# Optimization experiments

Measured on AMD Instinct MI355X. Metric: run time of the kernel, lower is better.

## Reference

```python
import jax, jax.numpy as jnp
import numpy as np

N = 50000
E = 800000
D = 128
EPS = 1e-5


def setup_inputs() -> dict:
    key = jax.random.key(0)
    ks = jax.random.split(key, 12)
    x = jax.random.normal(ks[0], (N, D), dtype=jnp.float32)
    pos = jax.random.normal(ks[1], (N, 3), dtype=jnp.float32)
    edge_index = jax.random.randint(ks[2], (2, E), 0, N, dtype=jnp.int32)
    s_e1 = 1.0 / np.sqrt(2 * D + 1)
    s_d = 1.0 / np.sqrt(D)
    s_n1 = 1.0 / np.sqrt(2 * D)
    return {
        "x": x,
        "pos": pos,
        "edge_index": edge_index,
        "W1e": jax.random.uniform(ks[3], (2 * D + 1, D), jnp.float32, -s_e1, s_e1),
        "b1e": jnp.zeros((D,), jnp.float32),
        "W2e": jax.random.uniform(ks[4], (D, D), jnp.float32, -s_d, s_d),
        "b2e": jnp.zeros((D,), jnp.float32),
        "W1n": jax.random.uniform(ks[5], (2 * D, D), jnp.float32, -s_n1, s_n1),
        "b1n": jnp.zeros((D,), jnp.float32),
        "W2n": jax.random.uniform(ks[6], (D, D), jnp.float32, -s_d, s_d),
        "b2n": jnp.zeros((D,), jnp.float32),
        "gamma": jnp.ones((D,), jnp.float32),
        "beta": jnp.zeros((D,), jnp.float32),
    }


def reference(x, pos, edge_index, W1e, b1e, W2e, b2e, W1n, b1n, W2n, b2n, gamma, beta):
    row, col = edge_index[0], edge_index[1]
    # gather + relative position
    rel_pos = pos[row] - pos[col]                       # [E, 3]
    dist2 = jnp.sum(rel_pos * rel_pos, axis=1, keepdims=True)  # [E, 1]
    edge_input = jnp.concatenate([x[row], x[col], dist2], axis=1)  # [E, 2D+1]
    # 2-layer edge MLP with SiLU activations
    h = jax.nn.silu(edge_input @ W1e + b1e)
    edge_feat = jax.nn.silu(h @ W2e + b2e)              # [E, D]
    # scatter-add aggregation onto source nodes (row)
    agg = jax.ops.segment_sum(edge_feat, row, num_segments=x.shape[0])  # [N, D]
    # 2-layer node MLP (SiLU only after first layer)
    node_in = jnp.concatenate([x, agg], axis=1)         # [N, 2D]
    update = jax.nn.silu(node_in @ W1n + b1n) @ W2n + b2n
    # dropout omitted (inference/eval mode)
    # LayerNorm(x + update)
    y = x + update
    mu = jnp.mean(y, axis=-1, keepdims=True)
    var = jnp.var(y, axis=-1, keepdims=True)
    return (y - mu) * jax.lax.rsqrt(var + EPS) * gamma + beta
```

## Files before the change

### kernel.cpp

```cpp
#include <hip/hip_runtime.h>
#include <hip/hip_bf16.h>
#include <math.h>

#define D 128
#define NND 50000
#define NE 800000
#define NB1 196
#define TPITCH 152
#define CPITCH 132

typedef __attribute__((ext_vector_type(8))) short shortx8;
typedef __attribute__((ext_vector_type(4))) float floatx4;

__device__ __forceinline__ float silu_f(float v) {
    return v * __builtin_amdgcn_rcpf(1.0f + __expf(-v));
}
__device__ __forceinline__ unsigned short f2bf(float f) {
    union { float f; unsigned int u; } v; v.f = f;
    unsigned int u = v.u;
    u += 0x7fffu + ((u >> 16) & 1u);
    return (unsigned short)(u >> 16);
}
__device__ __forceinline__ void unpk(unsigned int u, float& lo, float& hi) {
    union { unsigned int x; float f; } a, b;
    a.x = u << 16;
    b.x = u & 0xffff0000u;
    lo = a.f; hi = b.f;
}

__global__ void zero_kernel(float4* __restrict__ p, int n4) {
    int i = blockIdx.x * blockDim.x + threadIdx.x;
    float4 z = make_float4(0.f, 0.f, 0.f, 0.f);
    for (; i < n4; i += gridDim.x * blockDim.x) p[i] = z;
}

__global__ void hist_kernel(const int* __restrict__ ei, int* __restrict__ deg) {
    int e = blockIdx.x * 256 + threadIdx.x;
    atomicAdd(&deg[ei[e]], 1);
}

__global__ void scan1_kernel(const int* __restrict__ deg,
                             int* __restrict__ part, int* __restrict__ bsum) {
    __shared__ int s[256];
    const int tid = threadIdx.x;
    const int i = blockIdx.x * 256 + tid;
    int v = (i < NND) ? deg[i] : 0;
    s[tid] = v;
    __syncthreads();
    #pragma unroll
    for (int off = 1; off < 256; off <<= 1) {
        int t = (tid >= off) ? s[tid - off] : 0;
        __syncthreads();
        s[tid] += t;
        __syncthreads();
    }
    part[i] = s[tid] - v;
    if (tid == 255) bsum[blockIdx.x] = s[255];
}

__global__ void scan2_kernel(const int* __restrict__ bsum, int* __restrict__ boff) {
    __shared__ int s[256];
    const int tid = threadIdx.x;
    int v = (tid < NB1) ? bsum[tid] : 0;
    s[tid] = v;
    __syncthreads();
    #pragma unroll
    for (int off = 1; off < 256; off <<= 1) {
        int t = (tid >= off) ? s[tid - off] : 0;
        __syncthreads();
        s[tid] += t;
        __syncthreads();
    }
    if (tid < NB1) boff[tid] = s[tid] - v;
}

__global__ void scan3_kernel(const int* __restrict__ part, const int* __restrict__ boff,
                             int* __restrict__ rowptr, int* __restrict__ cursor) {
    int i = blockIdx.x * 256 + threadIdx.x;
    if (i < NND) {
        int v = part[i] + boff[i >> 8];
        rowptr[i] = v;
        cursor[i] = v;
    } else if (i == NND) {
        rowptr[NND] = NE;
    }
}

__global__ void scatter_kernel(const int* __restrict__ ei, const float* __restrict__ pos,
                               int* __restrict__ cursor,
                               uint4* __restrict__ epack) {
    int e = blockIdx.x * 256 + threadIdx.x;
    int r = ei[e], c = ei[NE + e];
    float dx = pos[r * 3 + 0] - pos[c * 3 + 0];
    float dy = pos[r * 3 + 1] - pos[c * 3 + 1];
    float dz = pos[r * 3 + 2] - pos[c * 3 + 2];
    float d2 = dx * dx + dy * dy + dz * dz;
    int slot = atomicAdd(&cursor[r], 1);
    uint4 v;
    v.x = (unsigned int)c;
    v.y = (unsigned int)r;
    v.z = __float_as_uint(d2);
    v.w = 0u;
    epack[slot] = v;
}

__global__ void wswzall_kernel(const float* __restrict__ W1e, const float* __restrict__ W1n,
                               const float* __restrict__ W2e, const float* __restrict__ W2n,
                               unsigned short* __restrict__ w1f, unsigned short* __restrict__ w1nf,
                               unsigned short* __restrict__ w2f, unsigned short* __restrict__ w2nf,
                               unsigned short* __restrict__ wlf) {
    const int b = blockIdx.x;
    const float* W; unsigned short* Wf; int lb;
    if (b < 128)      { W = W1e; Wf = w1f;  lb = b; }
    else if (b < 256) { W = W1n; Wf = w1nf; lb = b - 128; }
    else if (b < 320) { W = W2e; Wf = w2f;  lb = b - 256; }
    else if (b < 384) { W = W2n; Wf = w2nf; lb = b - 320; }
    else {
        if (threadIdx.x < 128) wlf[threadIdx.x] = f2bf(W1e[256 * D + threadIdx.x]);
        return;
    }
    int f = lb * 256 + threadIdx.x;
    int j    = f & 7;
    int mrow = (f >> 3) & 15;
    int n    = (f >> 7) & 7;
    int rest = f >> 10;
    int quad = rest & 3;
    int ks   = rest >> 2;
    int col = n * 16 + mrow;
    int k   = ks * 32 + quad * 8 + j;
    Wf[f] = f2bf(W[k * D + col]);
}

__global__ __launch_bounds__(256) void precompute_kernel(
        const float* __restrict__ x,
        const unsigned short* __restrict__ w1f,
        const float* __restrict__ b1e,
        unsigned short* __restrict__ A,
        unsigned short* __restrict__ Bm) {
    const int t    = threadIdx.x;
    const int wv   = t >> 6;
    const int lane = t & 63;
    const int mrow = lane & 15;
    const int quad = lane >> 4;
    const int tile = blockIdx.x * 4 + wv;
    if (tile >= 3125) return;
    const int n0 = tile * 16;

    const float4* xrow = (const float4*)(x + ((size_t)(n0 + mrow) << 7));
    const uint4* wp   = (const uint4*)w1f;

    floatx4 accA[8], accB[8];
    #pragma unroll
    for (int n = 0; n < 8; ++n) {
        accA[n] = (floatx4){0.f, 0.f, 0.f, 0.f};
        accB[n] = (floatx4){0.f, 0.f, 0.f, 0.f};
    }

    #pragma unroll
    for (int s = 0; s < 4; ++s) {
        float4 xa = xrow[(s * 4 + quad) * 2 + 0];
        float4 xb = xrow[(s * 4 + quad) * 2 + 1];
        union { shortx8 v; __hip_bfloat162 p[4]; } af;
        af.p[0] = __float22bfloat162_rn(float2{xa.x, xa.y});
        af.p[1] = __float22bfloat162_rn(float2{xa.z, xa.w});
        af.p[2] = __float22bfloat162_rn(float2{xb.x, xb.y});
        af.p[3] = __float22bfloat162_rn(float2{xb.z, xb.w});
        const int baseA = (s * 4 + quad) * 128 + mrow;
        const int baseB = ((s + 4) * 4 + quad) * 128 + mrow;
        #pragma unroll
        for (int n = 0; n < 8; ++n) {
            union { uint4 u; shortx8 v; } bfA, bfB;
            bfA.u = wp[baseA + n * 16];
            bfB.u = wp[baseB + n * 16];
            accA[n] = __builtin_amdgcn_mfma_f32_16x16x32_bf16(af.v, bfA.v, accA[n], 0, 0, 0);
            accB[n] = __builtin_amdgcn_mfma_f32_16x16x32_bf16(af.v, bfB.v, accB[n], 0, 0, 0);
        }
    }

    float bb[8];
    #pragma unroll
    for (int n = 0; n < 8; ++n) bb[n] = b1e[n * 16 + mrow];

    #pragma unroll
    for (int reg = 0; reg < 4; ++reg) {
        const int node = n0 + quad * 4 + reg;
        #pragma unroll
        for (int n = 0; n < 8; ++n) {
            const int col = n * 16 + mrow;
            A[(size_t)node * D + col]  = f2bf(accA[n][reg] + bb[n]);
            Bm[(size_t)node * D + col] = f2bf(accB[n][reg]);
        }
    }
}

__global__ __launch_bounds__(256, 2) void edgered_kernel(
        const unsigned short* __restrict__ Abf,
        const unsigned short* __restrict__ Bbf,
        const uint4* __restrict__ epack,
        const unsigned short* __restrict__ wlf,
        const unsigned short* __restrict__ W2f,
        const float* __restrict__ b2e,
        float* __restrict__ hpart,
        float* __restrict__ tpart,
        float* __restrict__ aggf) {
    __shared__ float cs[64][CPITCH];
    __shared__ int   rn[64];

    const int t    = threadIdx.x;
    const int wv   = t >> 6;
    const int lane = t & 63;
    const int mrow = lane & 15;
    const int quad = lane >> 4;
    const int e0   = blockIdx.x * 64 + wv * 16;
    const int eme  = e0 + mrow;

    const uint4 ep = epack[eme];
    const int   c  = (int)ep.x;
    const int   r  = (int)ep.y;
    const float d2 = __uint_as_float(ep.z);

    const uint4* arow = (const uint4*)(Abf + ((size_t)r << 7));
    const uint4* brow = (const uint4*)(Bbf + ((size_t)c << 7));
    const uint4* wlq  = (const uint4*)wlf;
    const uint4* w2p  = (const uint4*)W2f;

    uint4 au[4], bu[4], wu[4];
    #pragma unroll
    for (int s = 0; s < 4; ++s) {
        au[s] = arow[s * 4 + quad];
        bu[s] = brow[s * 4 + quad];
        wu[s] = wlq[s * 4 + quad];
    }

    floatx4 acc[8];
    #pragma unroll
    for (int k = 0; k < 8; ++k) acc[k] = (floatx4){0.f, 0.f, 0.f, 0.f};

    #pragma unroll
    for (int s = 0; s < 4; ++s) {
        float a0, a1, a2, a3, a4, a5, a6, a7;
        float q0, q1, q2, q3, q4, q5, q6, q7;
        float w0, w1, w2, w3, w4, w5, w6, w7;
        unpk(au[s].x, a0, a1); unpk(au[s].y, a2, a3);
        unpk(au[s].z, a4, a5); unpk(au[s].w, a6, a7);
        unpk(bu[s].x, q0, q1); unpk(bu[s].y, q2, q3);
        unpk(bu[s].z, q4, q5); unpk(bu[s].w, q6, q7);
        unpk(wu[s].x, w0, w1); unpk(wu[s].y, w2, w3);
        unpk(wu[s].z, w4, w5); unpk(wu[s].w, w6, w7);

        float h0 = silu_f(fmaf(d2, w0, a0 + q0));
        float h1 = silu_f(fmaf(d2, w1, a1 + q1));
        float h2 = silu_f(fmaf(d2, w2, a2 + q2));
        float h3 = silu_f(fmaf(d2, w3, a3 + q3));
        float h4 = silu_f(fmaf(d2, w4, a4 + q4));
        float h5 = silu_f(fmaf(d2, w5, a5 + q5));
        float h6 = silu_f(fmaf(d2, w6, a6 + q6));
        float h7 = silu_f(fmaf(d2, w7, a7 + q7));

        union { shortx8 v; __hip_bfloat162 p[4]; } af;
        af.p[0] = __float22bfloat162_rn(float2{h0, h1});
        af.p[1] = __float22bfloat162_rn(float2{h2, h3});
        af.p[2] = __float22bfloat162_rn(float2{h4, h5});
        af.p[3] = __float22bfloat162_rn(float2{h6, h7});

        const int base = (s * 4 + quad) * 128 + mrow;
        #pragma unroll
        for (int k = 0; k < 8; ++k) {
            union { uint4 u; shortx8 v; } bf;
            bf.u = w2p[base + k * 16];
            acc[k] = __builtin_amdgcn_mfma_f32_16x16x32_bf16(af.v, bf.v, acc[k], 0, 0, 0);
        }
    }

    float bias[8];
    #pragma unroll
    for (int k = 0; k < 8; ++k) bias[k] = b2e[k * 16 + mrow];

    #pragma unroll
    for (int reg = 0; reg < 4; ++reg) {
        const int row = wv * 16 + quad * 4 + reg;
        #pragma unroll
        for (int k = 0; k < 8; ++k)
            cs[row][k * 16 + mrow] = silu_f(acc[k][reg] + bias[k]);
    }
    if (lane < 16) rn[wv * 16 + lane] = r;
    __syncthreads();

    if (wv < 2) {
        const int col = wv * 64 + lane;
        const size_t blk = blockIdx.x;
        int i = 0;
        while (i < 64) {
            const int n = rn[i];
            int j = i + 1;
            while (j < 64 && rn[j] == n) ++j;
            float s = 0.f;
            for (int kk = i; kk < j; ++kk) s += cs[kk][col];
            if (i == 0)        hpart[blk * 128 + col] = s;
            else if (j == 64)  tpart[blk * 128 + col] = s;
            else               aggf[(size_t)n * 128 + col] = s;
            i = j;
        }
    }
}

__global__ __launch_bounds__(256) void combine_kernel(
        const float* __restrict__ hpart,
        const float* __restrict__ tpart,
        const int* __restrict__ rowptr,
        float* __restrict__ aggf) {
    const int lane = threadIdx.x & 63;
    const int node = blockIdx.x * 4 + (threadIdx.x >> 6);
    const int start = rowptr[node];
    const int end   = rowptr[node + 1];
    float2* ag2 = (float2*)(aggf + ((size_t)node << 7));
    const float2* h2 = (const float2*)hpart;
    const float2* t2 = (const float2*)tpart;

    if (start == end) { ag2[lane] = make_float2(0.f, 0.f); return; }
    const int t0 = start >> 6, t1 = (end - 1) >> 6;
    if (t0 == t1) {
        if ((start & 63) == 0)    ag2[lane] = h2[(size_t)t0 * 64 + lane];
        else if ((end & 63) == 0) ag2[lane] = t2[(size_t)t0 * 64 + lane];
        return;
    }
    float2 a = ((start & 63) == 0) ? h2[(size_t)t0 * 64 + lane]
                                   : t2[(size_t)t0 * 64 + lane];
    for (int tt = t0 + 1; tt < t1; ++tt) {
        float2 b = h2[(size_t)tt * 64 + lane];
        a.x += b.x; a.y += b.y;
    }
    float2 b = h2[(size_t)t1 * 64 + lane];
    a.x += b.x; a.y += b.y;
    ag2[lane] = a;
}

__global__ __launch_bounds__(64) void node_kernel(
        const float* __restrict__ aggf,
        const unsigned short* __restrict__ w1nf,
        const float* __restrict__ b1n,
        const unsigned short* __restrict__ w2nf,
        const float* __restrict__ b2n,
        const float* __restrict__ x,
        const float* __restrict__ gamma,
        const float* __restrict__ beta,
        float* __restrict__ out) {
    __shared__ __align__(16) unsigned short ts[16 * TPITCH];
    const int lane = threadIdx.x;
    const int mrow = lane & 15;
    const int quad = lane >> 4;
    const int n0 = blockIdx.x * 16;

    const float4* xrow  = (const float4*)(x + ((size_t)(n0 + mrow) << 7));
    const float4* growf = (const float4*)(aggf + ((size_t)(n0 + mrow) << 7));
    const uint4*  w1p   = (const uint4*)w1nf;
    const uint4*  w2p   = (const uint4*)w2nf;

    floatx4 acc[8];
    #pragma unroll
    for (int n = 0; n < 8; ++n) {
        float b = b1n[n * 16 + mrow];
        acc[n] = (floatx4){b, b, b, b};
    }

    #pragma unroll
    for (int s = 0; s < 4; ++s) {
        float4 xa = xrow[(s * 4 + quad) * 2 + 0];
        float4 xb = xrow[(s * 4 + quad) * 2 + 1];
        union { shortx8 v; __hip_bfloat162 p[4]; } af;
        af.p[0] = __float22bfloat162_rn(float2{xa.x, xa.y});
        af.p[1] = __float22bfloat162_rn(float2{xa.z, xa.w});
        af.p[2] = __float22bfloat162_rn(float2{xb.x, xb.y});
        af.p[3] = __float22bfloat162_rn(float2{xb.z, xb.w});
        const int base = (s * 4 + quad) * 128 + mrow;
        #pragma unroll
        for (int n = 0; n < 8; ++n) {
            union { uint4 u; shortx8 v; } bf;
            bf.u = w1p[base + n * 16];
            acc[n] = __builtin_amdgcn_mfma_f32_16x16x32_bf16(af.v, bf.v, acc[n], 0, 0, 0);
        }
    }
    #pragma unroll
    for (int s = 0; s < 4; ++s) {
        float4 g0 = growf[(s * 4 + quad) * 2 + 0];
        float4 g1 = growf[(s * 4 + quad) * 2 + 1];
        union { shortx8 v; __hip_bfloat162 p[4]; } af;
        af.p[0] = __float22bfloat162_rn(float2{g0.x, g0.y});
        af.p[1] = __float22bfloat162_rn(float2{g0.z, g0.w});
        af.p[2] = __float22bfloat162_rn(float2{g1.x, g1.y});
        af.p[3] = __float22bfloat162_rn(float2{g1.z, g1.w});
        const int base = ((s + 4) * 4 + quad) * 128 + mrow;
        #pragma unroll
        for (int n = 0; n < 8; ++n) {
            union { uint4 u; shortx8 v; } bf;
            bf.u = w1p[base + n * 16];
            acc[n] = __builtin_amdgcn_mfma_f32_16x16x32_bf16(af.v, bf.v, acc[n], 0, 0, 0);
        }
    }

    #pragma unroll
    for (int reg = 0; reg < 4; ++reg) {
        const int m = quad * 4 + reg;
        #pragma unroll
        for (int n = 0; n < 8; ++n)
            ts[m * TPITCH + n * 16 + mrow] = f2bf(silu_f(acc[n][reg]));
    }
    __syncthreads();

    floatx4 acc2[8];
    #pragma unroll
    for (int n = 0; n < 8; ++n) {
        float b = b2n[n * 16 + mrow];
        acc2[n] = (floatx4){b, b, b, b};
    }
    #pragma unroll
    for (int s = 0; s < 4; ++s) {
        shortx8 af2 = *(const shortx8*)((const char*)ts +
                        mrow * (TPITCH * 2) + (s * 4 + quad) * 16);
        const int base = (s * 4 + quad) * 128 + mrow;
        #pragma unroll
        for (int n = 0; n < 8; ++n) {
            union { uint4 u; shortx8 v; } bf;
            bf.u = w2p[base + n * 16];
            acc2[n] = __builtin_amdgcn_mfma_f32_16x16x32_bf16(af2, bf.v, acc2[n], 0, 0, 0);
        }
    }

    float g[8], bt[8];
    #pragma unroll
    for (int n = 0; n < 8; ++n) {
        g[n]  = gamma[n * 16 + mrow];
        bt[n] = beta[n * 16 + mrow];
    }
    #pragma unroll
    for (int reg = 0; reg < 4; ++reg) {
        const int node = n0 + quad * 4 + reg;
        float u[8];
        float s1 = 0.f, s2 = 0.f;
        #pragma unroll
        for (int n = 0; n < 8; ++n) {
            u[n] = acc2[n][reg] + x[(size_t)node * D + n * 16 + mrow];
            s1 += u[n];
            s2 += u[n] * u[n];
        }
        #pragma unroll
        for (int off = 1; off < 16; off <<= 1) {
            s1 += __shfl_xor(s1, off);
            s2 += __shfl_xor(s2, off);
        }
        const float mu  = s1 * (1.f / 128.f);
        const float var = s2 * (1.f / 128.f) - mu * mu;
        const float rs  = rsqrtf(var + 1e-5f);
        #pragma unroll
        for (int n = 0; n < 8; ++n)
            out[(size_t)node * D + n * 16 + mrow] = (u[n] - mu) * rs * g[n] + bt[n];
    }
}

extern "C" void kernel_launch(void* const* d_in, const int* in_sizes, int n_in,
                              void* d_out, int out_size, void* d_ws, size_t ws_size,
                              hipStream_t stream) {
    const float* x     = (const float*)d_in[0];
    const float* pos   = (const float*)d_in[1];
    const int*   ei    = (const int*)d_in[2];
    const float* W1e   = (const float*)d_in[3];
    const float* b1e   = (const float*)d_in[4];
    const float* W2e   = (const float*)d_in[5];
    const float* b2e   = (const float*)d_in[6];
    const float* W1n   = (const float*)d_in[7];
    const float* b1n   = (const float*)d_in[8];
    const float* W2n   = (const float*)d_in[9];
    const float* b2n   = (const float*)d_in[10];
    const float* gamma = (const float*)d_in[11];
    const float* beta  = (const float*)d_in[12];
    float* out = (float*)d_out;

    int*            deg    = (int*)d_ws;
    int*            part   = deg + 50176;
    int*            bsum   = part + 50176;
    int*            boff   = bsum + 256;
    int*            rowptr = boff + 256;
    int*            cursor = rowptr + 50004;
    uint4*          epack  = (uint4*)(cursor + 50000);
    unsigned short* Abf    = (unsigned short*)(epack + NE);
    unsigned short* Bbf    = Abf + (size_t)NND * D;
    unsigned short* w1f    = Bbf + (size_t)NND * D;
    unsigned short* w1nf   = w1f + 256 * D;
    unsigned short* w2f    = w1nf + 256 * D;
    unsigned short* w2nf   = w2f + D * D;
    unsigned short* wlf    = w2nf + D * D;
    float*          aggf   = (float*)(wlf + 128);
    float*          hpart  = aggf + (size_t)NND * D;
    float*          tpart  = hpart + (size_t)(NE / 64) * D;

    zero_kernel<<<49, 256, 0, stream>>>((float4*)deg, 50176 / 4);

    hist_kernel<<<NE / 256, 256, 0, stream>>>(ei, deg);
    scan1_kernel<<<NB1, 256, 0, stream>>>(deg, part, bsum);
    scan2_kernel<<<1, 256, 0, stream>>>(bsum, boff);
    scan3_kernel<<<197, 256, 0, stream>>>(part, boff, rowptr, cursor);
    scatter_kernel<<<NE / 256, 256, 0, stream>>>(ei, pos, cursor, epack);

    wswzall_kernel<<<385, 256, 0, stream>>>(W1e, W1n, W2e, W2n,
                                            w1f, w1nf, w2f, w2nf, wlf);

    precompute_kernel<<<782, 256, 0, stream>>>(x, w1f, b1e, Abf, Bbf);

    edgered_kernel<<<NE / 64, 256, 0, stream>>>(Abf, Bbf, epack, wlf, w2f, b2e,
                                                hpart, tpart, aggf);
    combine_kernel<<<NND / 4, 256, 0, stream>>>(hpart, tpart, rowptr, aggf);

    node_kernel<<<NND / 16, 64, 0, stream>>>(aggf, w1nf, b1n, w2nf, b2n,
                                             x, gamma, beta, out);
}
```

Measured before the change: 397.3 us.

## Reduce edge segments per wave in registers instead of via shared memory

The 64-edge block-level segmented reduction through a shared-memory tile and __syncthreads is replaced by a per-wave 16-edge reduction done in registers. Run boundaries come from a shuffle plus ballot, and each run is summed with cross-quad xor shuffles. This removes the LDS tile, the block barrier, and the serial loop on two waves. In exchange there are four times as many head/tail partial tiles, a larger workspace, more work in the combine kernel, and a shuffle-reduce loop per run, which costs more when a tile contains many distinct rows.

Result: faster. 347.4 us (-12.6%).

```diff
diff --git a/kernel.cpp b/kernel.cpp
--- a/kernel.cpp
+++ b/kernel.cpp
@@ -7,7 +7,6 @@
 #define NE 800000
 #define NB1 196
 #define TPITCH 152
-#define CPITCH 132
 
 typedef __attribute__((ext_vector_type(8))) short shortx8;
 typedef __attribute__((ext_vector_type(4))) float floatx4;
@@ -200,18 +199,16 @@
         const unsigned short* __restrict__ wlf,
         const unsigned short* __restrict__ W2f,
         const float* __restrict__ b2e,
-        float* __restrict__ hpart,
-        float* __restrict__ tpart,
+        float* __restrict__ hp,
+        float* __restrict__ tp,
         float* __restrict__ aggf) {
-    __shared__ float cs[64][CPITCH];
-    __shared__ int   rn[64];
-
     const int t    = threadIdx.x;
     const int wv   = t >> 6;
     const int lane = t & 63;
     const int mrow = lane & 15;
     const int quad = lane >> 4;
-    const int e0   = blockIdx.x * 64 + wv * 16;
+    const int tile = blockIdx.x * 4 + wv;
+    const int e0   = tile * 16;
     const int eme  = e0 + mrow;
 
     const uint4 ep = epack[eme];
@@ -277,36 +274,49 @@
     for (int k = 0; k < 8; ++k) bias[k] = b2e[k * 16 + mrow];
 
     #pragma unroll
-    for (int reg = 0; reg < 4; ++reg) {
-        const int row = wv * 16 + quad * 4 + reg;
-        #pragma unroll
-        for (int k = 0; k < 8; ++k)
-            cs[row][k * 16 + mrow] = silu_f(acc[k][reg] + bias[k]);
-    }
-    if (lane < 16) rn[wv * 16 + lane] = r;
-    __syncthreads();
-
-    if (wv < 2) {
-        const int col = wv * 64 + lane;
-        const size_t blk = blockIdx.x;
-        int i = 0;
-        while (i < 64) {
-            const int n = rn[i];
-            int j = i + 1;
-            while (j < 64 && rn[j] == n) ++j;
-            float s = 0.f;
-            for (int kk = i; kk < j; ++kk) s += cs[kk][col];
-            if (i == 0)        hpart[blk * 128 + col] = s;
-            else if (j == 64)  tpart[blk * 128 + col] = s;
-            else               aggf[(size_t)n * 128 + col] = s;
-            i = j;
-        }
+    for (int k = 0; k < 8; ++k) {
+        #pragma unroll
+        for (int reg = 0; reg < 4; ++reg)
+            acc[k][reg] = silu_f(acc[k][reg] + bias[k]);
+    }
+
+    const int rp = __shfl(r, (mrow - 1) & 15);
+    const bool newrun = (mrow == 0) || (r != rp);
+    const unsigned mask16 = (unsigned)(__ballot(newrun) & 0xffffull);
+
+    int i = 0;
+    while (i < 16) {
+        const unsigned rest = mask16 & ~((1u << (i + 1)) - 1u);
+        const int j = rest ? (int)__builtin_ctz(rest) : 16;
+        const int n = __shfl(r, i);
+        float s[8];
+        #pragma unroll
+        for (int k = 0; k < 8; ++k) {
+            float v = 0.f;
+            #pragma unroll
+            for (int reg = 0; reg < 4; ++reg) {
+                const int row = quad * 4 + reg;
+                v += (row >= i && row < j) ? acc[k][reg] : 0.f;
+            }
+            v += __shfl_xor(v, 16);
+            v += __shfl_xor(v, 32);
+            s[k] = v;
+        }
+        if (quad == 0) {
+            float* dst;
+            if (i == 0)       dst = hp + (size_t)tile * 128;
+            else if (j == 16) dst = tp + (size_t)tile * 128;
+            else              dst = aggf + (size_t)n * 128;
+            #pragma unroll
+            for (int k = 0; k < 8; ++k) dst[k * 16 + mrow] = s[k];
+        }
+        i = j;
     }
 }
 
 __global__ __launch_bounds__(256) void combine_kernel(
-        const float* __restrict__ hpart,
-        const float* __restrict__ tpart,
+        const float* __restrict__ hp,
+        const float* __restrict__ tp,
         const int* __restrict__ rowptr,
         float* __restrict__ aggf) {
     const int lane = threadIdx.x & 63;
@@ -314,24 +324,22 @@
     const int start = rowptr[node];
     const int end   = rowptr[node + 1];
     float2* ag2 = (float2*)(aggf + ((size_t)node << 7));
-    const float2* h2 = (const float2*)hpart;
-    const float2* t2 = (const float2*)tpart;
+    const float2* h2 = (const float2*)hp;
+    const float2* t2 = (const float2*)tp;
 
     if (start == end) { ag2[lane] = make_float2(0.f, 0.f); return; }
-    const int t0 = start >> 6, t1 = (end - 1) >> 6;
+    const int t0 = start >> 4, t1 = (end - 1) >> 4;
     if (t0 == t1) {
-        if ((start & 63) == 0)    ag2[lane] = h2[(size_t)t0 * 64 + lane];
-        else if ((end & 63) == 0) ag2[lane] = t2[(size_t)t0 * 64 + lane];
+        if ((start & 15) == 0)    ag2[lane] = h2[(size_t)t0 * 64 + lane];
+        else if ((end & 15) == 0) ag2[lane] = t2[(size_t)t0 * 64 + lane];
         return;
     }
-    float2 a = ((start & 63) == 0) ? h2[(size_t)t0 * 64 + lane]
+    float2 a = ((start & 15) == 0) ? h2[(size_t)t0 * 64 + lane]
                                    : t2[(size_t)t0 * 64 + lane];
-    for (int tt = t0 + 1; tt < t1; ++tt) {
+    for (int tt = t0 + 1; tt <= t1; ++tt) {
         float2 b = h2[(size_t)tt * 64 + lane];
         a.x += b.x; a.y += b.y;
     }
-    float2 b = h2[(size_t)t1 * 64 + lane];
-    a.x += b.x; a.y += b.y;
     ag2[lane] = a;
 }
 
@@ -490,8 +498,8 @@
     unsigned short* w2nf   = w2f + D * D;
     unsigned short* wlf    = w2nf + D * D;
     float*          aggf   = (float*)(wlf + 128);
-    float*          hpart  = aggf + (size_t)NND * D;
-    float*          tpart  = hpart + (size_t)(NE / 64) * D;
+    float*          hp     = aggf + (size_t)NND * D;
+    float*          tp     = hp + (size_t)(NE / 16) * D;
 
     zero_kernel<<<49, 256, 0, stream>>>((float4*)deg, 50176 / 4);
 
@@ -507,8 +515,8 @@
     precompute_kernel<<<782, 256, 0, stream>>>(x, w1f, b1e, Abf, Bbf);
 
     edgered_kernel<<<NE / 64, 256, 0, stream>>>(Abf, Bbf, epack, wlf, w2f, b2e,
-                                                hpart, tpart, aggf);
-    combine_kernel<<<NND / 4, 256, 0, stream>>>(hpart, tpart, rowptr, aggf);
+                                                hp, tp, aggf);
+    combine_kernel<<<NND / 4, 256, 0, stream>>>(hp, tp, rowptr, aggf);
 
     node_kernel<<<NND / 16, 64, 0, stream>>>(aggf, w1nf, b1n, w2nf, b2n,
                                              x, gamma, beta, out);
```
